# Optimization experiments

Measured on AMD Instinct MI355X. Metric: run time of the kernel, lower is better.

Reference implementation:

```python
import jax, jax.numpy as jnp
import numpy as np

N, BOND, PHYS = 784, 4, 2
BS = 16384
STD = 1e-08


def setup_inputs() -> dict:
    key = jax.random.key(0)
    k1, k2 = jax.random.split(key)
    data = jax.random.randint(k1, (BS, N), 0, 2).astype(jnp.float32)
    bias = jnp.eye(BOND, dtype=jnp.float32)[:, :, None].repeat(PHYS, axis=2)  # (BOND,BOND,PHYS)
    tensors = STD * jax.random.normal(k2, (N, BOND, BOND, PHYS), dtype=jnp.float32) + bias
    return {"data": data, "tensors": tensors}


def reference(data, tensors):
    # data: (bs, n) in {0,1}; tensors: (n, D, D, P)
    bs, n = data.shape
    emb = jnp.stack([data, 1.0 - data], axis=2)  # (bs, n, P)
    # per-site transfer matrices for every sample: (n, bs, D, D)
    mats = jnp.einsum('nlri,bni->nblr', tensors, emb)
    left0 = mats[0][:, 0, :]  # (bs, D)  -- row 0 of site-0 matrix
    lx0 = jax.nn.log_softmax(tensors[0, 0, 0])  # (P,)

    def step(left, xs):
        t, m = xs  # t: (D, D, P), m: (bs, D, D)
        logits = left @ t[:, 0, :]              # (bs, P)
        lx = jax.nn.log_softmax(logits, axis=1)  # (bs, P)
        new_left = jnp.einsum('bl,blr->br', left, m)
        return new_left, lx

    _, lxs = jax.lax.scan(step, left0, (tensors[1:], mats[1:]))  # (n-1, bs, P)
    logx = jnp.concatenate(
        [jnp.broadcast_to(lx0, (1, bs, PHYS)), lxs], axis=0)  # (n, bs, P)
    logx = jnp.transpose(logx, (1, 0, 2))  # (bs, n, P)
    log_prob = logx[..., 0] * data + logx[..., 1] * (1.0 - data)
    return log_prob.sum(-1)  # (bs,)
```

## Files before the change

### kernel.cpp

```cpp
#include <hip/hip_runtime.h>

#define NSITES 784
#define BS_TOT 16384
#define KSEG 16
#define GSEG 49
#define NQUAD 12
#define WPB  64

typedef unsigned long long u64;

#define STEP(sbit, TP) do {                                                          \
    const float* t_ = (TP);                                                          \
    float p00 = fmaf(left0, t_[0],  fmaf(left1, t_[8],  fmaf(left2, t_[16], left3 * t_[24]))); \
    float p01 = fmaf(left0, t_[1],  fmaf(left1, t_[9],  fmaf(left2, t_[17], left3 * t_[25]))); \
    float p10 = fmaf(left0, t_[2],  fmaf(left1, t_[10], fmaf(left2, t_[18], left3 * t_[26]))); \
    float p11 = fmaf(left0, t_[3],  fmaf(left1, t_[11], fmaf(left2, t_[19], left3 * t_[27]))); \
    float p20 = fmaf(left0, t_[4],  fmaf(left1, t_[12], fmaf(left2, t_[20], left3 * t_[28]))); \
    float p21 = fmaf(left0, t_[5],  fmaf(left1, t_[13], fmaf(left2, t_[21], left3 * t_[29]))); \
    float p30 = fmaf(left0, t_[6],  fmaf(left1, t_[14], fmaf(left2, t_[22], left3 * t_[30]))); \
    float p31 = fmaf(left0, t_[7],  fmaf(left1, t_[15], fmaf(left2, t_[23], left3 * t_[31]))); \
    bool s_ = (sbit);                                                                \
    float mx_ = fmaxf(p00, p01);                                                     \
    float ch_ = s_ ? p00 : p01;                                                      \
    acc_nat += (ch_ - mx_);                                                          \
    float ad_ = fabsf(p00 - p01);                                                    \
    acc_l2 += __builtin_amdgcn_logf(1.0f + __builtin_amdgcn_exp2f(-ad_ * 1.4426950408889634f)); \
    left0 = s_ ? p00 : p01;                                                          \
    left1 = s_ ? p10 : p11;                                                          \
    left2 = s_ ? p20 : p21;                                                          \
    left3 = s_ ? p30 : p31;                                                          \
} while (0)

#define MM_ROW(Q, Pr) do {                                                           \
    Q.x = fmaf(Pr.x, m0.x, fmaf(Pr.y, m1.x, fmaf(Pr.z, m2.x, Pr.w * m3.x)));         \
    Q.y = fmaf(Pr.x, m0.y, fmaf(Pr.y, m1.y, fmaf(Pr.z, m2.y, Pr.w * m3.y)));         \
    Q.z = fmaf(Pr.x, m0.z, fmaf(Pr.y, m1.z, fmaf(Pr.z, m2.z, Pr.w * m3.z)));         \
    Q.w = fmaf(Pr.x, m0.w, fmaf(Pr.y, m1.w, fmaf(Pr.z, m2.w, Pr.w * m3.w)));         \
} while (0)

#define MM4(P0,P1,P2,P3) do { float4 Q0,Q1,Q2,Q3; \
    MM_ROW(Q0,P0); MM_ROW(Q1,P1); MM_ROW(Q2,P2); MM_ROW(Q3,P3); \
    P0=Q0; P1=Q1; P2=Q2; P3=Q3; } while (0)

__global__ __launch_bounds__(256) void pp_qq_kernel(const float* __restrict__ tensors,
                                                    float* __restrict__ QQ) {
    __shared__ float sPP[24][4][16];
    const int k = blockIdx.x;
    const int t = threadIdx.x;
    const int n0 = k * GSEG;

    if (t < 96) {
        const int j = t >> 2, c2 = t & 3;
        const float* t0 = tensors + (size_t)(n0 + 2 * j) * 32;
        const float* t1 = tensors + (size_t)(n0 + 2 * j + 1) * 32;
        const int p0 = (c2 & 1) ? 0 : 1;
        const int p1 = (c2 & 2) ? 0 : 1;
        float A[4][4], B[4][4];
        #pragma unroll
        for (int l = 0; l < 4; ++l)
            #pragma unroll
            for (int r = 0; r < 4; ++r) {
                A[l][r] = t0[l * 8 + r * 2 + p0];
                B[l][r] = t1[l * 8 + r * 2 + p1];
            }
        #pragma unroll
        for (int a = 0; a < 4; ++a)
            #pragma unroll
            for (int bb = 0; bb < 4; ++bb)
                sPP[j][c2][a * 4 + bb] =
                    fmaf(A[a][0], B[0][bb], fmaf(A[a][1], B[1][bb],
                    fmaf(A[a][2], B[2][bb], A[a][3] * B[3][bb])));
    }
    __syncthreads();

    if (t < 192) {
        const int q = t >> 4, c = t & 15;
        const float* A = sPP[2 * q][c & 3];
        const float* B = sPP[2 * q + 1][(c >> 2) & 3];
        float* dst = QQ + ((size_t)(k * NQUAD + q) * 16 + c) * 16;
        #pragma unroll
        for (int a = 0; a < 4; ++a)
            #pragma unroll
            for (int bb = 0; bb < 4; ++bb)
                dst[a * 4 + bb] =
                    fmaf(A[a * 4 + 0], B[0 * 4 + bb], fmaf(A[a * 4 + 1], B[1 * 4 + bb],
                    fmaf(A[a * 4 + 2], B[2 * 4 + bb], A[a * 4 + 3] * B[3 * 4 + bb])));
    }
}

__global__ __launch_bounds__(256) void pack_kernel(const float* __restrict__ data,
                                                   u64* __restrict__ packed) {
    int gid  = blockIdx.x * 256 + threadIdx.x;
    int row  = gid >> 6;
    int lane = threadIdx.x & 63;
    const float* r = data + (size_t)row * NSITES;
    #pragma unroll
    for (int w = 0; w < 12; ++w) {
        u64 m = __ballot(r[w * 64 + lane] == 1.0f);
        if (lane == 0) packed[(size_t)w * BS_TOT + row] = m;
    }
    float v = (lane < 16) ? r[768 + lane] : 0.0f;
    u64 m = __ballot((lane < 16) && (v == 1.0f));
    if (lane == 0) packed[(size_t)12 * BS_TOT + row] = m;
}

__device__ __forceinline__ u64 bit_window(const u64* __restrict__ packed, int n0, int b) {
    int a0 = n0 >> 6, s = n0 & 63;
    u64 w0 = packed[(size_t)a0 * BS_TOT + b];
    u64 w1 = packed[(size_t)(a0 + 1) * BS_TOT + b];
    return s ? ((w0 >> s) | (w1 << (64 - s))) : w0;
}

__global__ __launch_bounds__(256) void phase1q_kernel(const float* __restrict__ tensors,
                                                      const u64* __restrict__ packed,
                                                      const float* __restrict__ QQ,
                                                      float* __restrict__ Pbuf) {
    const int b = blockIdx.x * 256 + threadIdx.x;
    const int k = blockIdx.y;
    const int n0 = k * GSEG;

    __shared__ __align__(16) float lt[NQUAD * 16 * 20];
    {
        const float4* src = (const float4*)(QQ + (size_t)k * NQUAD * 16 * 16);
        float4* dst = (float4*)lt;
        for (int e = threadIdx.x; e < NQUAD * 16 * 4; e += 256) {
            int q = e >> 6, c = (e >> 2) & 15, j = e & 3;
            dst[q * 80 + c * 5 + j] = src[e];
        }
    }
    __syncthreads();

    u64 win = bit_window(packed, n0, b);
    const float4* ltf4 = (const float4*)lt;

    float4 P0, P1, P2, P3;
    {
        const int c0 = (int)(win & 15ull);
        const float4* mi = ltf4 + (c0 * 5);
        P0 = mi[0]; P1 = mi[1]; P2 = mi[2]; P3 = mi[3];
    }
    #pragma unroll
    for (int q = 1; q < NQUAD; ++q) {
        const int cq = (int)((win >> (4 * q)) & 15ull);
        const float4* mi = ltf4 + (q * 80 + cq * 5);
        float4 m0 = mi[0], m1 = mi[1], m2 = mi[2], m3 = mi[3];
        MM4(P0, P1, P2, P3);
    }
    {
        const float* t48 = tensors + (size_t)(n0 + 48) * 32;
        const bool s48 = ((win >> 48) & 1ull) != 0;
        float4 m0 = make_float4(s48 ? t48[0]  : t48[1],  s48 ? t48[2]  : t48[3],
                                s48 ? t48[4]  : t48[5],  s48 ? t48[6]  : t48[7]);
        float4 m1 = make_float4(s48 ? t48[8]  : t48[9],  s48 ? t48[10] : t48[11],
                                s48 ? t48[12] : t48[13], s48 ? t48[14] : t48[15]);
        float4 m2 = make_float4(s48 ? t48[16] : t48[17], s48 ? t48[18] : t48[19],
                                s48 ? t48[20] : t48[21], s48 ? t48[22] : t48[23]);
        float4 m3 = make_float4(s48 ? t48[24] : t48[25], s48 ? t48[26] : t48[27],
                                s48 ? t48[28] : t48[29], s48 ? t48[30] : t48[31]);
        MM4(P0, P1, P2, P3);
    }

    float4* pb = (float4*)(Pbuf + ((size_t)k * BS_TOT + b) * 16);
    pb[0] = P0; pb[1] = P1; pb[2] = P2; pb[3] = P3;
}

__global__ __launch_bounds__(1024, 4) void scan_walk_kernel(
    const float* __restrict__ tensors,
    const u64* __restrict__ packed,
    const float* __restrict__ Pbuf,
    float* __restrict__ out)
{
    __shared__ float sPre[KSEG][4][WPB];
    __shared__ float sRes[KSEG][WPB];

    const int t    = threadIdx.x;
    const int wv   = t >> 6;
    const int lane = t & 63;
    const int s0   = blockIdx.x * WPB;
    const int b    = s0 + lane;

    if (wv == 0) {
        float l0 = 1.0f, l1 = 0.0f, l2 = 0.0f, l3 = 0.0f;
        const float4* base = (const float4*)Pbuf + (size_t)b * 4;
        #pragma unroll
        for (int kc = 0; kc < 3; ++kc) {
            float4 R[5][4];
            #pragma unroll
            for (int j = 0; j < 5; ++j) {
                const float4* pb = base + (size_t)(kc * 5 + j) * BS_TOT * 4;
                R[j][0] = pb[0]; R[j][1] = pb[1]; R[j][2] = pb[2]; R[j][3] = pb[3];
            }
            #pragma unroll
            for (int j = 0; j < 5; ++j) {
                const int k = kc * 5 + j;
                sPre[k][0][lane] = l0; sPre[k][1][lane] = l1;
                sPre[k][2][lane] = l2; sPre[k][3][lane] = l3;
                float n0 = fmaf(l0, R[j][0].x, fmaf(l1, R[j][1].x, fmaf(l2, R[j][2].x, l3 * R[j][3].x)));
                float n1 = fmaf(l0, R[j][0].y, fmaf(l1, R[j][1].y, fmaf(l2, R[j][2].y, l3 * R[j][3].y)));
                float n2 = fmaf(l0, R[j][0].z, fmaf(l1, R[j][1].z, fmaf(l2, R[j][2].z, l3 * R[j][3].z)));
                float n3 = fmaf(l0, R[j][0].w, fmaf(l1, R[j][1].w, fmaf(l2, R[j][2].w, l3 * R[j][3].w)));
                l0 = n0; l1 = n1; l2 = n2; l3 = n3;
            }
        }
        sPre[15][0][lane] = l0; sPre[15][1][lane] = l1;
        sPre[15][2][lane] = l2; sPre[15][3][lane] = l3;
    }
    __syncthreads();

    {
        const int k  = wv;
        const int n0 = k * GSEG;
        u64 win = bit_window(packed, n0, b);

        const int n0u = __builtin_amdgcn_readfirstlane(n0);
        const float* tb = tensors + (size_t)n0u * 32;

        float left0 = sPre[k][0][lane], left1 = sPre[k][1][lane];
        float left2 = sPre[k][2][lane], left3 = sPre[k][3][lane];
        float acc_nat = 0.0f, acc_l2 = 0.0f;
        #pragma unroll 7
        for (int i = 0; i < GSEG; ++i) {
            STEP(((win >> i) & 1ull) != 0, tb + i * 32);
        }
        sRes[k][lane] = acc_nat - 0.6931471805599453f * acc_l2;
    }
    __syncthreads();

    if (wv == 0) {
        float acc = 0.0f;
        #pragma unroll
        for (int kk = 0; kk < KSEG; ++kk) acc += sRes[kk][lane];
        out[b] = acc;
    }
}

__global__ __launch_bounds__(64) void amps_chain_kernel(
    const float* __restrict__ data, const float* __restrict__ tensors,
    float* __restrict__ out)
{
    int b = blockIdx.x * blockDim.x + threadIdx.x;
    if (b >= BS_TOT) return;
    const float* row = data + (size_t)b * NSITES;
    float left0 = 1.0f, left1 = 0.0f, left2 = 0.0f, left3 = 0.0f;
    float acc_nat = 0.0f, acc_l2 = 0.0f;
    for (int n = 0; n < NSITES; ++n) {
        STEP(row[n] == 1.0f, tensors + (size_t)n * 32);
    }
    out[b] = acc_nat - 0.6931471805599453f * acc_l2;
}

extern "C" void kernel_launch(void* const* d_in, const int* in_sizes, int n_in,
                              void* d_out, int out_size, void* d_ws, size_t ws_size,
                              hipStream_t stream) {
    const float* data    = (const float*)d_in[0];
    const float* tensors = (const float*)d_in[1];
    float* out = (float*)d_out;

    const size_t packed_bytes = (size_t)13 * BS_TOT * 8;
    const size_t Pbuf_bytes   = (size_t)(KSEG - 1) * BS_TOT * 16 * 4;
    const size_t QQ_bytes     = (size_t)KSEG * NQUAD * 16 * 16 * 4;
    const size_t need = packed_bytes + Pbuf_bytes + QQ_bytes;

    if (ws_size < need) {
        hipLaunchKernelGGL(amps_chain_kernel, dim3(BS_TOT / 64), dim3(64), 0, stream,
                           data, tensors, out);
        return;
    }

    char* wsb = (char*)d_ws;
    u64*   packed = (u64*)wsb;
    float* Pbuf   = (float*)(wsb + packed_bytes);
    float* QQ     = (float*)(wsb + packed_bytes + Pbuf_bytes);

    hipLaunchKernelGGL(pp_qq_kernel,     dim3(KSEG), dim3(256), 0, stream, tensors, QQ);
    hipLaunchKernelGGL(pack_kernel,      dim3((BS_TOT * 64) / 256), dim3(256), 0, stream,
                       data, packed);
    hipLaunchKernelGGL(phase1q_kernel,   dim3(BS_TOT / 256, KSEG - 1), dim3(256), 0, stream,
                       tensors, packed, QQ, Pbuf);
    hipLaunchKernelGGL(scan_walk_kernel, dim3(BS_TOT / WPB), dim3(1024), 0, stream,
                       tensors, packed, Pbuf, out);
}
```

Measured before the change: 55.96 us.

## Split scan_walk into scan, dual-sample walk and reduce kernels; fuse pre-kernels

Merges the tensor-product precompute and bit-packing kernels into one launch, branching on block index. Replaces the monolithic 1024-thread scan_walk kernel with three kernels: a per-sample prefix scan that writes to global memory, a walk kernel where each thread processes two samples for ILP with a 2D grid over segments, and a final reduction. This aims to remove the serialized wave-0 scan bottleneck inside each block and to raise ILP. In exchange it adds global round-trips for prefix and partial results plus an extra launch.

```diff
diff --git a/kernel.cpp b/kernel.cpp
--- a/kernel.cpp
+++ b/kernel.cpp
@@ -5,31 +5,32 @@
 #define KSEG 16
 #define GSEG 49
 #define NQUAD 12
-#define WPB  64
 
 typedef unsigned long long u64;
 
-#define STEP(sbit, TP) do {                                                          \
+#define STEPV(sbit, TP, L0,L1,L2,L3, AN, AL) do {                                    \
     const float* t_ = (TP);                                                          \
-    float p00 = fmaf(left0, t_[0],  fmaf(left1, t_[8],  fmaf(left2, t_[16], left3 * t_[24]))); \
-    float p01 = fmaf(left0, t_[1],  fmaf(left1, t_[9],  fmaf(left2, t_[17], left3 * t_[25]))); \
-    float p10 = fmaf(left0, t_[2],  fmaf(left1, t_[10], fmaf(left2, t_[18], left3 * t_[26]))); \
-    float p11 = fmaf(left0, t_[3],  fmaf(left1, t_[11], fmaf(left2, t_[19], left3 * t_[27]))); \
-    float p20 = fmaf(left0, t_[4],  fmaf(left1, t_[12], fmaf(left2, t_[20], left3 * t_[28]))); \
-    float p21 = fmaf(left0, t_[5],  fmaf(left1, t_[13], fmaf(left2, t_[21], left3 * t_[29]))); \
-    float p30 = fmaf(left0, t_[6],  fmaf(left1, t_[14], fmaf(left2, t_[22], left3 * t_[30]))); \
-    float p31 = fmaf(left0, t_[7],  fmaf(left1, t_[15], fmaf(left2, t_[23], left3 * t_[31]))); \
+    float p00 = fmaf(L0, t_[0],  fmaf(L1, t_[8],  fmaf(L2, t_[16], L3 * t_[24])));   \
+    float p01 = fmaf(L0, t_[1],  fmaf(L1, t_[9],  fmaf(L2, t_[17], L3 * t_[25])));   \
+    float p10 = fmaf(L0, t_[2],  fmaf(L1, t_[10], fmaf(L2, t_[18], L3 * t_[26])));   \
+    float p11 = fmaf(L0, t_[3],  fmaf(L1, t_[11], fmaf(L2, t_[19], L3 * t_[27])));   \
+    float p20 = fmaf(L0, t_[4],  fmaf(L1, t_[12], fmaf(L2, t_[20], L3 * t_[28])));   \
+    float p21 = fmaf(L0, t_[5],  fmaf(L1, t_[13], fmaf(L2, t_[21], L3 * t_[29])));   \
+    float p30 = fmaf(L0, t_[6],  fmaf(L1, t_[14], fmaf(L2, t_[22], L3 * t_[30])));   \
+    float p31 = fmaf(L0, t_[7],  fmaf(L1, t_[15], fmaf(L2, t_[23], L3 * t_[31])));   \
     bool s_ = (sbit);                                                                \
     float mx_ = fmaxf(p00, p01);                                                     \
     float ch_ = s_ ? p00 : p01;                                                      \
-    acc_nat += (ch_ - mx_);                                                          \
+    AN += (ch_ - mx_);                                                               \
     float ad_ = fabsf(p00 - p01);                                                    \
-    acc_l2 += __builtin_amdgcn_logf(1.0f + __builtin_amdgcn_exp2f(-ad_ * 1.4426950408889634f)); \
-    left0 = s_ ? p00 : p01;                                                          \
-    left1 = s_ ? p10 : p11;                                                          \
-    left2 = s_ ? p20 : p21;                                                          \
-    left3 = s_ ? p30 : p31;                                                          \
+    AL += __builtin_amdgcn_logf(1.0f + __builtin_amdgcn_exp2f(-ad_ * 1.4426950408889634f)); \
+    L0 = s_ ? p00 : p01;                                                             \
+    L1 = s_ ? p10 : p11;                                                             \
+    L2 = s_ ? p20 : p21;                                                             \
+    L3 = s_ ? p30 : p31;                                                             \
 } while (0)
+
+#define STEP(sbit, TP) STEPV(sbit, TP, left0,left1,left2,left3, acc_nat, acc_l2)
 
 #define MM_ROW(Q, Pr) do {                                                           \
     Q.x = fmaf(Pr.x, m0.x, fmaf(Pr.y, m1.x, fmaf(Pr.z, m2.x, Pr.w * m3.x)));         \
@@ -42,66 +43,67 @@
     MM_ROW(Q0,P0); MM_ROW(Q1,P1); MM_ROW(Q2,P2); MM_ROW(Q3,P3); \
     P0=Q0; P1=Q1; P2=Q2; P3=Q3; } while (0)
 
-__global__ __launch_bounds__(256) void pp_qq_kernel(const float* __restrict__ tensors,
-                                                    float* __restrict__ QQ) {
-    __shared__ float sPP[24][4][16];
-    const int k = blockIdx.x;
-    const int t = threadIdx.x;
-    const int n0 = k * GSEG;
-
-    if (t < 96) {
-        const int j = t >> 2, c2 = t & 3;
-        const float* t0 = tensors + (size_t)(n0 + 2 * j) * 32;
-        const float* t1 = tensors + (size_t)(n0 + 2 * j + 1) * 32;
-        const int p0 = (c2 & 1) ? 0 : 1;
-        const int p1 = (c2 & 2) ? 0 : 1;
-        float A[4][4], B[4][4];
+__global__ __launch_bounds__(256) void fused_pre_kernel(const float* __restrict__ tensors,
+                                                        const float* __restrict__ data,
+                                                        float* __restrict__ QQ,
+                                                        u64* __restrict__ packed) {
+    if (blockIdx.x < KSEG) {
+        __shared__ float sPP[24][4][16];
+        const int k = blockIdx.x;
+        const int t = threadIdx.x;
+        const int n0 = k * GSEG;
+
+        if (t < 96) {
+            const int j = t >> 2, c2 = t & 3;
+            const float* t0 = tensors + (size_t)(n0 + 2 * j) * 32;
+            const float* t1 = tensors + (size_t)(n0 + 2 * j + 1) * 32;
+            const int p0 = (c2 & 1) ? 0 : 1;
+            const int p1 = (c2 & 2) ? 0 : 1;
+            float A[4][4], B[4][4];
+            #pragma unroll
+            for (int l = 0; l < 4; ++l)
+                #pragma unroll
+                for (int r = 0; r < 4; ++r) {
+                    A[l][r] = t0[l * 8 + r * 2 + p0];
+                    B[l][r] = t1[l * 8 + r * 2 + p1];
+                }
+            #pragma unroll
+            for (int a = 0; a < 4; ++a)
+                #pragma unroll
+                for (int bb = 0; bb < 4; ++bb)
+                    sPP[j][c2][a * 4 + bb] =
+                        fmaf(A[a][0], B[0][bb], fmaf(A[a][1], B[1][bb],
+                        fmaf(A[a][2], B[2][bb], A[a][3] * B[3][bb])));
+        }
+        __syncthreads();
+
+        if (t < 192) {
+            const int q = t >> 4, c = t & 15;
+            const float* A = sPP[2 * q][c & 3];
+            const float* B = sPP[2 * q + 1][(c >> 2) & 3];
+            float* dst = QQ + ((size_t)(k * NQUAD + q) * 16 + c) * 16;
+            #pragma unroll
+            for (int a = 0; a < 4; ++a)
+                #pragma unroll
+                for (int bb = 0; bb < 4; ++bb)
+                    dst[a * 4 + bb] =
+                        fmaf(A[a * 4 + 0], B[0 * 4 + bb], fmaf(A[a * 4 + 1], B[1 * 4 + bb],
+                        fmaf(A[a * 4 + 2], B[2 * 4 + bb], A[a * 4 + 3] * B[3 * 4 + bb])));
+        }
+    } else {
+        int gid  = (blockIdx.x - KSEG) * 256 + threadIdx.x;
+        int row  = gid >> 6;
+        int lane = threadIdx.x & 63;
+        const float* r = data + (size_t)row * NSITES;
         #pragma unroll
-        for (int l = 0; l < 4; ++l)
-            #pragma unroll
-            for (int r = 0; r < 4; ++r) {
-                A[l][r] = t0[l * 8 + r * 2 + p0];
-                B[l][r] = t1[l * 8 + r * 2 + p1];
-            }
-        #pragma unroll
-        for (int a = 0; a < 4; ++a)
-            #pragma unroll
-            for (int bb = 0; bb < 4; ++bb)
-                sPP[j][c2][a * 4 + bb] =
-                    fmaf(A[a][0], B[0][bb], fmaf(A[a][1], B[1][bb],
-                    fmaf(A[a][2], B[2][bb], A[a][3] * B[3][bb])));
-    }
-    __syncthreads();
-
-    if (t < 192) {
-        const int q = t >> 4, c = t & 15;
-        const float* A = sPP[2 * q][c & 3];
-        const float* B = sPP[2 * q + 1][(c >> 2) & 3];
-        float* dst = QQ + ((size_t)(k * NQUAD + q) * 16 + c) * 16;
-        #pragma unroll
-        for (int a = 0; a < 4; ++a)
-            #pragma unroll
-            for (int bb = 0; bb < 4; ++bb)
-                dst[a * 4 + bb] =
-                    fmaf(A[a * 4 + 0], B[0 * 4 + bb], fmaf(A[a * 4 + 1], B[1 * 4 + bb],
-                    fmaf(A[a * 4 + 2], B[2 * 4 + bb], A[a * 4 + 3] * B[3 * 4 + bb])));
-    }
-}
-
-__global__ __launch_bounds__(256) void pack_kernel(const float* __restrict__ data,
-                                                   u64* __restrict__ packed) {
-    int gid  = blockIdx.x * 256 + threadIdx.x;
-    int row  = gid >> 6;
-    int lane = threadIdx.x & 63;
-    const float* r = data + (size_t)row * NSITES;
-    #pragma unroll
-    for (int w = 0; w < 12; ++w) {
-        u64 m = __ballot(r[w * 64 + lane] == 1.0f);
-        if (lane == 0) packed[(size_t)w * BS_TOT + row] = m;
-    }
-    float v = (lane < 16) ? r[768 + lane] : 0.0f;
-    u64 m = __ballot((lane < 16) && (v == 1.0f));
-    if (lane == 0) packed[(size_t)12 * BS_TOT + row] = m;
+        for (int w = 0; w < 12; ++w) {
+            u64 m = __ballot(r[w * 64 + lane] == 1.0f);
+            if (lane == 0) packed[(size_t)w * BS_TOT + row] = m;
+        }
+        float v = (lane < 16) ? r[768 + lane] : 0.0f;
+        u64 m = __ballot((lane < 16) && (v == 1.0f));
+        if (lane == 0) packed[(size_t)12 * BS_TOT + row] = m;
+    }
 }
 
 __device__ __forceinline__ u64 bit_window(const u64* __restrict__ packed, int n0, int b) {
@@ -164,74 +166,79 @@
     pb[0] = P0; pb[1] = P1; pb[2] = P2; pb[3] = P3;
 }
 
-__global__ __launch_bounds__(1024, 4) void scan_walk_kernel(
-    const float* __restrict__ tensors,
-    const u64* __restrict__ packed,
-    const float* __restrict__ Pbuf,
-    float* __restrict__ out)
-{
-    __shared__ float sPre[KSEG][4][WPB];
-    __shared__ float sRes[KSEG][WPB];
-
-    const int t    = threadIdx.x;
-    const int wv   = t >> 6;
-    const int lane = t & 63;
-    const int s0   = blockIdx.x * WPB;
-    const int b    = s0 + lane;
-
-    if (wv == 0) {
-        float l0 = 1.0f, l1 = 0.0f, l2 = 0.0f, l3 = 0.0f;
-        const float4* base = (const float4*)Pbuf + (size_t)b * 4;
+__global__ __launch_bounds__(256) void scan_kernel(const float* __restrict__ Pbuf,
+                                                   float* __restrict__ prefix) {
+    int b = blockIdx.x * 256 + threadIdx.x;
+    float l0 = 1.0f, l1 = 0.0f, l2 = 0.0f, l3 = 0.0f;
+    const float4* base = (const float4*)Pbuf + (size_t)b * 4;
+    #pragma unroll
+    for (int kc = 0; kc < 3; ++kc) {
+        float4 R[5][4];
         #pragma unroll
-        for (int kc = 0; kc < 3; ++kc) {
-            float4 R[5][4];
-            #pragma unroll
-            for (int j = 0; j < 5; ++j) {
-                const float4* pb = base + (size_t)(kc * 5 + j) * BS_TOT * 4;
-                R[j][0] = pb[0]; R[j][1] = pb[1]; R[j][2] = pb[2]; R[j][3] = pb[3];
-            }
-            #pragma unroll
-            for (int j = 0; j < 5; ++j) {
-                const int k = kc * 5 + j;
-                sPre[k][0][lane] = l0; sPre[k][1][lane] = l1;
-                sPre[k][2][lane] = l2; sPre[k][3][lane] = l3;
-                float n0 = fmaf(l0, R[j][0].x, fmaf(l1, R[j][1].x, fmaf(l2, R[j][2].x, l3 * R[j][3].x)));
-                float n1 = fmaf(l0, R[j][0].y, fmaf(l1, R[j][1].y, fmaf(l2, R[j][2].y, l3 * R[j][3].y)));
-                float n2 = fmaf(l0, R[j][0].z, fmaf(l1, R[j][1].z, fmaf(l2, R[j][2].z, l3 * R[j][3].z)));
-                float n3 = fmaf(l0, R[j][0].w, fmaf(l1, R[j][1].w, fmaf(l2, R[j][2].w, l3 * R[j][3].w)));
-                l0 = n0; l1 = n1; l2 = n2; l3 = n3;
-            }
-        }
-        sPre[15][0][lane] = l0; sPre[15][1][lane] = l1;
-        sPre[15][2][lane] = l2; sPre[15][3][lane] = l3;
-    }
-    __syncthreads();
-
-    {
-        const int k  = wv;
-        const int n0 = k * GSEG;
-        u64 win = bit_window(packed, n0, b);
-
-        const int n0u = __builtin_amdgcn_readfirstlane(n0);
-        const float* tb = tensors + (size_t)n0u * 32;
-
-        float left0 = sPre[k][0][lane], left1 = sPre[k][1][lane];
-        float left2 = sPre[k][2][lane], left3 = sPre[k][3][lane];
-        float acc_nat = 0.0f, acc_l2 = 0.0f;
-        #pragma unroll 7
-        for (int i = 0; i < GSEG; ++i) {
-            STEP(((win >> i) & 1ull) != 0, tb + i * 32);
-        }
-        sRes[k][lane] = acc_nat - 0.6931471805599453f * acc_l2;
-    }
-    __syncthreads();
-
-    if (wv == 0) {
-        float acc = 0.0f;
+        for (int j = 0; j < 5; ++j) {
+            const float4* pb = base + (size_t)(kc * 5 + j) * BS_TOT * 4;
+            R[j][0] = pb[0]; R[j][1] = pb[1]; R[j][2] = pb[2]; R[j][3] = pb[3];
+        }
         #pragma unroll
-        for (int kk = 0; kk < KSEG; ++kk) acc += sRes[kk][lane];
-        out[b] = acc;
-    }
+        for (int j = 0; j < 5; ++j) {
+            const int k = kc * 5 + j;
+            prefix[((size_t)k * 4 + 0) * BS_TOT + b] = l0;
+            prefix[((size_t)k * 4 + 1) * BS_TOT + b] = l1;
+            prefix[((size_t)k * 4 + 2) * BS_TOT + b] = l2;
+            prefix[((size_t)k * 4 + 3) * BS_TOT + b] = l3;
+            float n0 = fmaf(l0, R[j][0].x, fmaf(l1, R[j][1].x, fmaf(l2, R[j][2].x, l3 * R[j][3].x)));
+            float n1 = fmaf(l0, R[j][0].y, fmaf(l1, R[j][1].y, fmaf(l2, R[j][2].y, l3 * R[j][3].y)));
+            float n2 = fmaf(l0, R[j][0].z, fmaf(l1, R[j][1].z, fmaf(l2, R[j][2].z, l3 * R[j][3].z)));
+            float n3 = fmaf(l0, R[j][0].w, fmaf(l1, R[j][1].w, fmaf(l2, R[j][2].w, l3 * R[j][3].w)));
+            l0 = n0; l1 = n1; l2 = n2; l3 = n3;
+        }
+    }
+    prefix[((size_t)15 * 4 + 0) * BS_TOT + b] = l0;
+    prefix[((size_t)15 * 4 + 1) * BS_TOT + b] = l1;
+    prefix[((size_t)15 * 4 + 2) * BS_TOT + b] = l2;
+    prefix[((size_t)15 * 4 + 3) * BS_TOT + b] = l3;
+}
+
+__global__ __launch_bounds__(256) void walk2_kernel(const float* __restrict__ tensors,
+                                                    const u64* __restrict__ packed,
+                                                    const float* __restrict__ prefix,
+                                                    float* __restrict__ res) {
+    const int k  = blockIdx.y;
+    const int n0 = k * GSEG;
+    const int b0 = blockIdx.x * 256 + threadIdx.x;
+    const int b1 = b0 + BS_TOT / 2;
+    const float* tb = tensors + (size_t)n0 * 32;
+
+    u64 winA = bit_window(packed, n0, b0);
+    u64 winB = bit_window(packed, n0, b1);
+
+    float lA0 = prefix[((size_t)k * 4 + 0) * BS_TOT + b0];
+    float lA1 = prefix[((size_t)k * 4 + 1) * BS_TOT + b0];
+    float lA2 = prefix[((size_t)k * 4 + 2) * BS_TOT + b0];
+    float lA3 = prefix[((size_t)k * 4 + 3) * BS_TOT + b0];
+    float lB0 = prefix[((size_t)k * 4 + 0) * BS_TOT + b1];
+    float lB1 = prefix[((size_t)k * 4 + 1) * BS_TOT + b1];
+    float lB2 = prefix[((size_t)k * 4 + 2) * BS_TOT + b1];
+    float lB3 = prefix[((size_t)k * 4 + 3) * BS_TOT + b1];
+    float anA = 0.0f, alA = 0.0f, anB = 0.0f, alB = 0.0f;
+
+    #pragma unroll 4
+    for (int i = 0; i < GSEG; ++i) {
+        const float* ts = tb + i * 32;
+        STEPV(((winA >> i) & 1ull) != 0, ts, lA0,lA1,lA2,lA3, anA, alA);
+        STEPV(((winB >> i) & 1ull) != 0, ts, lB0,lB1,lB2,lB3, anB, alB);
+    }
+    res[(size_t)k * BS_TOT + b0] = anA - 0.6931471805599453f * alA;
+    res[(size_t)k * BS_TOT + b1] = anB - 0.6931471805599453f * alB;
+}
+
+__global__ __launch_bounds__(256) void reduce_kernel(const float* __restrict__ res,
+                                                     float* __restrict__ out) {
+    int b = blockIdx.x * 256 + threadIdx.x;
+    float a = 0.0f;
+    #pragma unroll
+    for (int k = 0; k < KSEG; ++k) a += res[(size_t)k * BS_TOT + b];
+    out[b] = a;
 }
 
 __global__ __launch_bounds__(64) void amps_chain_kernel(
@@ -259,7 +266,9 @@
     const size_t packed_bytes = (size_t)13 * BS_TOT * 8;
     const size_t Pbuf_bytes   = (size_t)(KSEG - 1) * BS_TOT * 16 * 4;
     const size_t QQ_bytes     = (size_t)KSEG * NQUAD * 16 * 16 * 4;
-    const size_t need = packed_bytes + Pbuf_bytes + QQ_bytes;
+    const size_t prefix_bytes = (size_t)KSEG * 4 * BS_TOT * 4;
+    const size_t res_bytes    = (size_t)KSEG * BS_TOT * 4;
+    const size_t need = packed_bytes + Pbuf_bytes + QQ_bytes + prefix_bytes + res_bytes;
 
     if (ws_size < need) {
         hipLaunchKernelGGL(amps_chain_kernel, dim3(BS_TOT / 64), dim3(64), 0, stream,
@@ -271,12 +280,16 @@
     u64*   packed = (u64*)wsb;
     float* Pbuf   = (float*)(wsb + packed_bytes);
     float* QQ     = (float*)(wsb + packed_bytes + Pbuf_bytes);
-
-    hipLaunchKernelGGL(pp_qq_kernel,     dim3(KSEG), dim3(256), 0, stream, tensors, QQ);
-    hipLaunchKernelGGL(pack_kernel,      dim3((BS_TOT * 64) / 256), dim3(256), 0, stream,
-                       data, packed);
+    float* prefix = (float*)(wsb + packed_bytes + Pbuf_bytes + QQ_bytes);
+    float* res    = (float*)(wsb + packed_bytes + Pbuf_bytes + QQ_bytes + prefix_bytes);
+
+    hipLaunchKernelGGL(fused_pre_kernel, dim3(KSEG + (BS_TOT * 64) / 256), dim3(256), 0, stream,
+                       tensors, data, QQ, packed);
     hipLaunchKernelGGL(phase1q_kernel,   dim3(BS_TOT / 256, KSEG - 1), dim3(256), 0, stream,
                        tensors, packed, QQ, Pbuf);
-    hipLaunchKernelGGL(scan_walk_kernel, dim3(BS_TOT / WPB), dim3(1024), 0, stream,
-                       tensors, packed, Pbuf, out);
-}
+    hipLaunchKernelGGL(scan_kernel,      dim3(BS_TOT / 256), dim3(256), 0, stream,
+                       Pbuf, prefix);
+    hipLaunchKernelGGL(walk2_kernel,     dim3(BS_TOT / 2 / 256, KSEG), dim3(256), 0, stream,
+                       tensors, packed, prefix, res);
+    hipLaunchKernelGGL(reduce_kernel,    dim3(BS_TOT / 256), dim3(256), 0, stream, res, out);
+}
```

Measured after the change: 65.43 us. +16.9%, slower.
